# Optimization experiments

Measured on AMD Instinct MI355X. Metric: run time of the kernel, lower is better.

Reference implementation:

```python
import jax, jax.numpy as jnp
import numpy as np

TEMP = 1.0

def setup_inputs() -> dict:
    key = jax.random.key(0)
    k1, k2, k3 = jax.random.split(key, 3)
    B, C, H, W = 8, 256, 64, 64
    h = jax.random.normal(k1, (B, C, H, W), dtype=jnp.float32)
    xs = jax.random.normal(k2, (B, C, H, W), dtype=jnp.float32)
    ys = jax.random.normal(k3, (B, C, H, W), dtype=jnp.float32)
    return {"h": h, "xs": xs, "ys": ys}

def reference(h, xs, ys):
    B, C, H, W = h.shape
    Bs, Cs, Hs, Ws = xs.shape
    hf = h.reshape(B, C, H * W)            # [B, C, N]   N = H*W
    xf = xs.reshape(Bs, Cs, Hs * Ws)       # [B, C, M]   M = Hs*Ws
    yf = ys.reshape(ys.shape[0], ys.shape[1], -1)  # [B, C, M]
    # attention[b, n, m] = sum_c h[b,c,n] * xs[b,c,m]
    attn = jnp.einsum('bcn,bcm->bnm', hf, xf)
    attn = jax.nn.softmax(attn / TEMP, axis=2)  # softmax over support positions m
    # xxs[b, c, n] = sum_m ys[b,c,m] * attn[b,n,m]
    xxs = jnp.einsum('bcm,bnm->bcn', yf, attn)
    return xxs.reshape(B, C, H, W)
```

## Files before the change

### kernel.cpp

```cpp
#include <hip/hip_runtime.h>
#include <stdint.h>

#define B_ 8
#define C_ 256
#define N_ 4096
#define M_ 4096
#define NT 64
#define MT 64
#define PP 72
#define L2E 1.44269504f

typedef _Float16 f16x8 __attribute__((ext_vector_type(8)));
typedef _Float16 f16x4 __attribute__((ext_vector_type(4)));
typedef float f32x4 __attribute__((ext_vector_type(4)));

__device__ __forceinline__ void async16(const _Float16* g, _Float16* l) {
    __builtin_amdgcn_global_load_lds(
        (const __attribute__((address_space(1))) void*)g,
        (__attribute__((address_space(3))) void*)l, 16, 0, 0);
}

__global__ __launch_bounds__(256) void kPre(const float* __restrict__ xs,
                                            const float* __restrict__ ys,
                                            _Float16* __restrict__ kt,
                                            _Float16* __restrict__ vb) {
    int bx = blockIdx.x;
    int t = threadIdx.x;
    if (bx < 2048) {
        __shared__ float tile[64][65];
        int b = bx >> 8, rem = bx & 255;
        int c0 = (rem >> 6) * 64, m0 = (rem & 63) * 64;
        int cl = t >> 4, m4 = (t & 15) * 4;
#pragma unroll
        for (int i = 0; i < 4; i++) {
            int c = c0 + cl + i * 16;
            const float4 v = *(const float4*)(xs + ((size_t)(b * C_ + c) * M_) + m0 + m4);
            tile[m4 + 0][cl + i * 16] = v.x;
            tile[m4 + 1][cl + i * 16] = v.y;
            tile[m4 + 2][cl + i * 16] = v.z;
            tile[m4 + 3][cl + i * 16] = v.w;
        }
        __syncthreads();
        int ml = t >> 4, c4 = (t & 15) * 4;
#pragma unroll
        for (int i = 0; i < 4; i++) {
            int m = m0 + ml + i * 16;
            f16x4 o;
            o[0] = (_Float16)tile[ml + i * 16][c4 + 0];
            o[1] = (_Float16)tile[ml + i * 16][c4 + 1];
            o[2] = (_Float16)tile[ml + i * 16][c4 + 2];
            o[3] = (_Float16)tile[ml + i * 16][c4 + 3];
            *(f16x4*)(kt + ((size_t)(b * M_ + m) * C_) + c0 + c4) = o;
        }
    } else {
        size_t i = ((size_t)(bx - 2048) * 256 + t) * 4;
        float4 v = *(const float4*)(ys + i);
        f16x4 o;
        o[0] = (_Float16)v.x; o[1] = (_Float16)v.y;
        o[2] = (_Float16)v.z; o[3] = (_Float16)v.w;
        *(f16x4*)(vb + i) = o;
    }
}

__global__ __launch_bounds__(256, 2) void kAttn(const float* __restrict__ h,
                                                const _Float16* __restrict__ kt,
                                                const _Float16* __restrict__ vb,
                                                float* __restrict__ out) {
    __shared__ _Float16 sK[2][MT * 256];
    __shared__ _Float16 sP[NT * PP];
    __shared__ float sAlpha[NT];
    __shared__ float sL[NT];
    __shared__ int sFlag[2];

    const int t = threadIdx.x;
    const int w = t >> 6, lane = t & 63, quad = lane >> 4, l15 = lane & 15;
    const int b = blockIdx.x >> 6;
    const int n0 = (blockIdx.x & 63) * NT;
    const int nb = w * 16;
    const int cb = w * 64;

    const _Float16* srcKb = kt + (size_t)b * M_ * C_;
    const _Float16* srcVb = vb + (size_t)b * C_ * M_;

    if (t == 0) { sFlag[0] = 0; sFlag[1] = 0; }

    {
        int cl = t >> 4, n4 = (t & 15) * 4;
        for (int i = 0; i < 16; i++) {
            int c = i * 16 + cl;
            const float4 v = *(const float4*)(h + ((size_t)(b * C_ + c) * N_) + n0 + n4);
            float xv[4] = {v.x, v.y, v.z, v.w};
#pragma unroll
            for (int j = 0; j < 4; j++) {
                int row = n4 + j;
                sK[1][row * 256 + (((c >> 3) ^ (row & 31)) << 3) + (c & 7)] = (_Float16)xv[j];
            }
        }
#pragma unroll
        for (int j = 0; j < 8; j++) {
            int row = w * 16 + j * 2 + (lane >> 5);
            int logi = (lane & 31) ^ (row & 31);
            async16(srcKb + (size_t)row * C_ + logi * 8, &sK[0][(w * 16 + j * 2) * 256]);
        }
    }
    asm volatile("s_waitcnt lgkmcnt(0)" ::: "memory");
    __builtin_amdgcn_s_barrier();

    f16x8 qf[8];
    {
        int qrow = nb + l15;
#pragma unroll
        for (int ks = 0; ks < 8; ks++)
            qf[ks] = *(const f16x8*)(&sK[1][qrow * 256 + ((((ks << 2) + quad) ^ (qrow & 31)) << 3)]);
    }
    asm volatile("s_waitcnt lgkmcnt(0)" ::: "memory");

    f32x4 o[4][4];
#pragma unroll
    for (int i = 0; i < 4; i++)
#pragma unroll
        for (int j = 0; j < 4; j++)
            o[i][j] = (f32x4){0.f, 0.f, 0.f, 0.f};

    float mst = -3.0e38f, lp = 0.f;

    for (int it = 0; it < M_ / MT; it++) {
        const int cur = it & 1, nxt = cur ^ 1;
        const int m0i = it * MT;
        asm volatile("s_waitcnt vmcnt(0)" ::: "memory");
        __builtin_amdgcn_s_barrier();

        if (t == 0) sFlag[nxt] = 0;

        f16x8 vf[2][4];
#pragma unroll
        for (int ks = 0; ks < 2; ks++)
#pragma unroll
            for (int ct = 0; ct < 4; ct++) {
                int vrow = cb + ct * 16 + l15;
                vf[ks][ct] = *(const f16x8*)(srcVb + (size_t)vrow * M_ + m0i + ks * 32 + quad * 8);
            }
        __builtin_amdgcn_sched_barrier(0);

        if (it + 1 < M_ / MT) {
            const _Float16* srcK = srcKb + (size_t)(m0i + MT) * C_;
#pragma unroll
            for (int j = 0; j < 8; j++) {
                int row = w * 16 + j * 2 + (lane >> 5);
                int logi = (lane & 31) ^ (row & 31);
                async16(srcK + (size_t)row * C_ + logi * 8, &sK[nxt][(w * 16 + j * 2) * 256]);
            }
        }

        f32x4 s[4];
#pragma unroll
        for (int mt = 0; mt < 4; mt++) s[mt] = (f32x4){0.f, 0.f, 0.f, 0.f};
        __builtin_amdgcn_s_setprio(1);
#pragma unroll
        for (int ks = 0; ks < 8; ks++) {
#pragma unroll
            for (int mt = 0; mt < 4; mt++) {
                int krow = mt * 16 + l15;
                f16x8 bk = *(const f16x8*)(&sK[cur][krow * 256 + ((((ks << 2) + quad) ^ (krow & 31)) << 3)]);
                s[mt] = __builtin_amdgcn_mfma_f32_16x16x32_f16(bk, qf[ks], s[mt], 0, 0, 0);
            }
        }
        __builtin_amdgcn_s_setprio(0);

        float rowmax = fmaxf(fmaxf(fmaxf(s[0][0], s[0][1]), fmaxf(s[0][2], s[0][3])),
                             fmaxf(fmaxf(s[1][0], s[1][1]), fmaxf(s[1][2], s[1][3])));
        rowmax = fmaxf(rowmax, fmaxf(fmaxf(fmaxf(s[2][0], s[2][1]), fmaxf(s[2][2], s[2][3])),
                                     fmaxf(fmaxf(s[3][0], s[3][1]), fmaxf(s[3][2], s[3][3]))));
        rowmax = fmaxf(rowmax, __shfl_xor(rowmax, 16, 64));
        rowmax = fmaxf(rowmax, __shfl_xor(rowmax, 32, 64));
        float al = 1.0f;
        if (rowmax > mst) {
            al = exp2f((mst - rowmax) * L2E);
            mst = rowmax;
        }
        const float mb = mst * L2E;
        float psum = 0.f;
#pragma unroll
        for (int mt = 0; mt < 4; mt++)
#pragma unroll
            for (int r = 0; r < 4; r++) {
                float p = exp2f(s[mt][r] * L2E - mb);
                s[mt][r] = p;
                psum += p;
            }
        lp = lp * al + psum;
        if (quad == 0) {
            sAlpha[nb + l15] = al;
            if (al != 1.0f) atomicOr(&sFlag[cur], 1);
        }
#pragma unroll
        for (int mt = 0; mt < 4; mt++) {
            f16x4 pk;
            pk[0] = (_Float16)s[mt][0];
            pk[1] = (_Float16)s[mt][1];
            pk[2] = (_Float16)s[mt][2];
            pk[3] = (_Float16)s[mt][3];
            *(f16x4*)(&sP[(nb + l15) * PP + mt * 16 + quad * 4]) = pk;
        }

        asm volatile("s_waitcnt lgkmcnt(0)" ::: "memory");
        __builtin_amdgcn_s_barrier();

        if (sFlag[cur]) {
            float av[4];
#pragma unroll
            for (int nt = 0; nt < 4; nt++) av[nt] = sAlpha[nt * 16 + l15];
#pragma unroll
            for (int ct = 0; ct < 4; ct++)
#pragma unroll
                for (int nt = 0; nt < 4; nt++) {
                    o[ct][nt][0] *= av[nt];
                    o[ct][nt][1] *= av[nt];
                    o[ct][nt][2] *= av[nt];
                    o[ct][nt][3] *= av[nt];
                }
        }

        __builtin_amdgcn_s_setprio(1);
#pragma unroll
        for (int ks = 0; ks < 2; ks++) {
#pragma unroll
            for (int nt = 0; nt < 4; nt++) {
                f16x8 bp = *(const f16x8*)(sP + (nt * 16 + l15) * PP + ks * 32 + quad * 8);
#pragma unroll
                for (int ct = 0; ct < 4; ct++)
                    o[ct][nt] = __builtin_amdgcn_mfma_f32_16x16x32_f16(vf[ks][ct], bp, o[ct][nt], 0, 0, 0);
            }
        }
        __builtin_amdgcn_s_setprio(0);
    }

    lp += __shfl_xor(lp, 16, 64);
    lp += __shfl_xor(lp, 32, 64);
    if (quad == 0) sL[nb + l15] = lp;
    __syncthreads();
    float linv[4];
#pragma unroll
    for (int nt = 0; nt < 4; nt++) linv[nt] = 1.0f / sL[nt * 16 + l15];
#pragma unroll
    for (int ct = 0; ct < 4; ct++)
#pragma unroll
        for (int nt = 0; nt < 4; nt++)
#pragma unroll
            for (int r = 0; r < 4; r++) {
                int c = cb + ct * 16 + quad * 4 + r;
                out[((size_t)(b * C_ + c)) * N_ + n0 + nt * 16 + l15] = o[ct][nt][r] * linv[nt];
            }
}

extern "C" void kernel_launch(void* const* d_in, const int* in_sizes, int n_in,
                              void* d_out, int out_size, void* d_ws, size_t ws_size,
                              hipStream_t stream) {
    const float* h  = (const float*)d_in[0];
    const float* xs = (const float*)d_in[1];
    const float* ys = (const float*)d_in[2];
    float* out = (float*)d_out;

    _Float16* kt  = (_Float16*)d_ws;
    _Float16* vbb = kt + (size_t)B_ * M_ * C_;

    kPre<<<dim3(2048 + 8192), 256, 0, stream>>>(xs, ys, kt, vbb);
    kAttn<<<dim3(B_ * (N_ / NT)), 256, 0, stream>>>(h, kt, vbb, out);
}
```

Measured before the change: 361.2 us.

## Split attention into producer and consumer waves with one-step software pipeline

Doubles the block to 8 waves: four waves compute QK^T scores and online softmax for a 32-key tile while four other waves apply rescaling and the PV MFMA for the previous tile. Q is moved from registers to LDS, the key tile shrinks from 64 to 32, and the block-to-batch mapping is interleaved. The intent is to overlap softmax/score work with the PV accumulation and raise occupancy, at the cost of twice as many barriers per key and more LDS pressure.

Result: slower. 503.5 us (+39.4%).

```diff
diff --git a/kernel.cpp b/kernel.cpp
--- a/kernel.cpp
+++ b/kernel.cpp
@@ -6,8 +6,9 @@
 #define N_ 4096
 #define M_ 4096
 #define NT 64
-#define MT 64
-#define PP 72
+#define MT 32
+#define MITER (M_ / MT)
+#define PP 40
 #define L2E 1.44269504f
 
 typedef _Float16 f16x8 __attribute__((ext_vector_type(8)));
@@ -62,11 +63,12 @@
     }
 }
 
-__global__ __launch_bounds__(256, 2) void kAttn(const float* __restrict__ h,
+__global__ __launch_bounds__(512, 4) void kAttn(const float* __restrict__ h,
                                                 const _Float16* __restrict__ kt,
                                                 const _Float16* __restrict__ vb,
                                                 float* __restrict__ out) {
     __shared__ _Float16 sK[2][MT * 256];
+    __shared__ _Float16 sQ[NT * 256];
     __shared__ _Float16 sP[NT * PP];
     __shared__ float sAlpha[NT];
     __shared__ float sL[NT];
@@ -74,46 +76,39 @@
 
     const int t = threadIdx.x;
     const int w = t >> 6, lane = t & 63, quad = lane >> 4, l15 = lane & 15;
-    const int b = blockIdx.x >> 6;
-    const int n0 = (blockIdx.x & 63) * NT;
-    const int nb = w * 16;
-    const int cb = w * 64;
+    const int b = blockIdx.x & 7;
+    const int n0 = (blockIdx.x >> 3) * NT;
+    const bool prod = (w < 4);
+    const int pw = w & 3;
+    const int nb = pw * 16;
+    const int cb = pw * 64;
 
     const _Float16* srcKb = kt + (size_t)b * M_ * C_;
     const _Float16* srcVb = vb + (size_t)b * C_ * M_;
 
     if (t == 0) { sFlag[0] = 0; sFlag[1] = 0; }
 
+#pragma unroll
+    for (int j = 0; j < 2; j++) {
+        int row = w * 4 + j * 2 + (lane >> 5);
+        int logi = (lane & 31) ^ (row & 31);
+        async16(srcKb + (size_t)row * C_ + logi * 8, &sK[0][(w * 4 + j * 2) * 256]);
+    }
     {
-        int cl = t >> 4, n4 = (t & 15) * 4;
-        for (int i = 0; i < 16; i++) {
-            int c = i * 16 + cl;
+        int cl = t >> 4;
+        int n4 = (t & 15) * 4;
+#pragma unroll
+        for (int i = 0; i < 8; i++) {
+            int c = i * 32 + cl;
             const float4 v = *(const float4*)(h + ((size_t)(b * C_ + c) * N_) + n0 + n4);
             float xv[4] = {v.x, v.y, v.z, v.w};
 #pragma unroll
             for (int j = 0; j < 4; j++) {
                 int row = n4 + j;
-                sK[1][row * 256 + (((c >> 3) ^ (row & 31)) << 3) + (c & 7)] = (_Float16)xv[j];
-            }
-        }
-#pragma unroll
-        for (int j = 0; j < 8; j++) {
-            int row = w * 16 + j * 2 + (lane >> 5);
-            int logi = (lane & 31) ^ (row & 31);
-            async16(srcKb + (size_t)row * C_ + logi * 8, &sK[0][(w * 16 + j * 2) * 256]);
-        }
-    }
-    asm volatile("s_waitcnt lgkmcnt(0)" ::: "memory");
-    __builtin_amdgcn_s_barrier();
-
-    f16x8 qf[8];
-    {
-        int qrow = nb + l15;
-#pragma unroll
-        for (int ks = 0; ks < 8; ks++)
-            qf[ks] = *(const f16x8*)(&sK[1][qrow * 256 + ((((ks << 2) + quad) ^ (qrow & 31)) << 3)]);
-    }
-    asm volatile("s_waitcnt lgkmcnt(0)" ::: "memory");
+                sQ[row * 256 + (((c >> 3) ^ (row & 31)) << 3) + (c & 7)] = (_Float16)xv[j];
+            }
+        }
+    }
 
     f32x4 o[4][4];
 #pragma unroll
@@ -121,136 +116,143 @@
 #pragma unroll
         for (int j = 0; j < 4; j++)
             o[i][j] = (f32x4){0.f, 0.f, 0.f, 0.f};
-
+    f16x8 vf[4];
     float mst = -3.0e38f, lp = 0.f;
-
-    for (int it = 0; it < M_ / MT; it++) {
+    float al = 1.0f;
+    f32x4 s4[2];
+
+    for (int it = 0; it <= MITER; it++) {
         const int cur = it & 1, nxt = cur ^ 1;
-        const int m0i = it * MT;
-        asm volatile("s_waitcnt vmcnt(0)" ::: "memory");
+        asm volatile("s_waitcnt vmcnt(0) lgkmcnt(0)" ::: "memory");
         __builtin_amdgcn_s_barrier();
 
-        if (t == 0) sFlag[nxt] = 0;
-
-        f16x8 vf[2][4];
-#pragma unroll
-        for (int ks = 0; ks < 2; ks++)
-#pragma unroll
-            for (int ct = 0; ct < 4; ct++) {
-                int vrow = cb + ct * 16 + l15;
-                vf[ks][ct] = *(const f16x8*)(srcVb + (size_t)vrow * M_ + m0i + ks * 32 + quad * 8);
-            }
-        __builtin_amdgcn_sched_barrier(0);
-
-        if (it + 1 < M_ / MT) {
-            const _Float16* srcK = srcKb + (size_t)(m0i + MT) * C_;
-#pragma unroll
-            for (int j = 0; j < 8; j++) {
-                int row = w * 16 + j * 2 + (lane >> 5);
+        if (it < MITER - 1) {
+            const _Float16* srcK = srcKb + (size_t)(it + 1) * MT * C_;
+#pragma unroll
+            for (int j = 0; j < 2; j++) {
+                int row = w * 4 + j * 2 + (lane >> 5);
                 int logi = (lane & 31) ^ (row & 31);
-                async16(srcK + (size_t)row * C_ + logi * 8, &sK[nxt][(w * 16 + j * 2) * 256]);
-            }
-        }
-
-        f32x4 s[4];
-#pragma unroll
-        for (int mt = 0; mt < 4; mt++) s[mt] = (f32x4){0.f, 0.f, 0.f, 0.f};
-        __builtin_amdgcn_s_setprio(1);
-#pragma unroll
-        for (int ks = 0; ks < 8; ks++) {
-#pragma unroll
-            for (int mt = 0; mt < 4; mt++) {
-                int krow = mt * 16 + l15;
-                f16x8 bk = *(const f16x8*)(&sK[cur][krow * 256 + ((((ks << 2) + quad) ^ (krow & 31)) << 3)]);
-                s[mt] = __builtin_amdgcn_mfma_f32_16x16x32_f16(bk, qf[ks], s[mt], 0, 0, 0);
-            }
-        }
-        __builtin_amdgcn_s_setprio(0);
-
-        float rowmax = fmaxf(fmaxf(fmaxf(s[0][0], s[0][1]), fmaxf(s[0][2], s[0][3])),
-                             fmaxf(fmaxf(s[1][0], s[1][1]), fmaxf(s[1][2], s[1][3])));
-        rowmax = fmaxf(rowmax, fmaxf(fmaxf(fmaxf(s[2][0], s[2][1]), fmaxf(s[2][2], s[2][3])),
-                                     fmaxf(fmaxf(s[3][0], s[3][1]), fmaxf(s[3][2], s[3][3]))));
-        rowmax = fmaxf(rowmax, __shfl_xor(rowmax, 16, 64));
-        rowmax = fmaxf(rowmax, __shfl_xor(rowmax, 32, 64));
-        float al = 1.0f;
-        if (rowmax > mst) {
-            al = exp2f((mst - rowmax) * L2E);
-            mst = rowmax;
-        }
-        const float mb = mst * L2E;
-        float psum = 0.f;
-#pragma unroll
-        for (int mt = 0; mt < 4; mt++)
-#pragma unroll
-            for (int r = 0; r < 4; r++) {
-                float p = exp2f(s[mt][r] * L2E - mb);
-                s[mt][r] = p;
-                psum += p;
-            }
-        lp = lp * al + psum;
-        if (quad == 0) {
-            sAlpha[nb + l15] = al;
-            if (al != 1.0f) atomicOr(&sFlag[cur], 1);
-        }
-#pragma unroll
-        for (int mt = 0; mt < 4; mt++) {
-            f16x4 pk;
-            pk[0] = (_Float16)s[mt][0];
-            pk[1] = (_Float16)s[mt][1];
-            pk[2] = (_Float16)s[mt][2];
-            pk[3] = (_Float16)s[mt][3];
-            *(f16x4*)(&sP[(nb + l15) * PP + mt * 16 + quad * 4]) = pk;
+                async16(srcK + (size_t)row * C_ + logi * 8, &sK[nxt][(w * 4 + j * 2) * 256]);
+            }
+        }
+
+        if (prod) {
+            if (it < MITER) {
+                s4[0] = (f32x4){0.f, 0.f, 0.f, 0.f};
+                s4[1] = (f32x4){0.f, 0.f, 0.f, 0.f};
+                const int qrow = nb + l15;
+                __builtin_amdgcn_s_setprio(1);
+#pragma unroll
+                for (int ks = 0; ks < 8; ks++) {
+                    f16x8 qk = *(const f16x8*)(&sQ[qrow * 256 + ((((ks << 2) + quad) ^ (qrow & 31)) << 3)]);
+#pragma unroll
+                    for (int mt = 0; mt < 2; mt++) {
+                        int krow = mt * 16 + l15;
+                        f16x8 bk = *(const f16x8*)(&sK[cur][krow * 256 + ((((ks << 2) + quad) ^ (krow & 31)) << 3)]);
+                        s4[mt] = __builtin_amdgcn_mfma_f32_16x16x32_f16(bk, qk, s4[mt], 0, 0, 0);
+                    }
+                }
+                __builtin_amdgcn_s_setprio(0);
+
+                float rowmax = fmaxf(fmaxf(fmaxf(s4[0][0], s4[0][1]), fmaxf(s4[0][2], s4[0][3])),
+                                     fmaxf(fmaxf(s4[1][0], s4[1][1]), fmaxf(s4[1][2], s4[1][3])));
+                rowmax = fmaxf(rowmax, __shfl_xor(rowmax, 16, 64));
+                rowmax = fmaxf(rowmax, __shfl_xor(rowmax, 32, 64));
+                al = 1.0f;
+                if (rowmax > mst) {
+                    al = exp2f((mst - rowmax) * L2E);
+                    mst = rowmax;
+                }
+                const float mb = mst * L2E;
+                float psum = 0.f;
+#pragma unroll
+                for (int mt = 0; mt < 2; mt++)
+#pragma unroll
+                    for (int r = 0; r < 4; r++) {
+                        float p = exp2f(s4[mt][r] * L2E - mb);
+                        s4[mt][r] = p;
+                        psum += p;
+                    }
+                lp = lp * al + psum;
+            }
+        } else {
+            if (it > 0 && sFlag[nxt]) {
+                float av[4];
+#pragma unroll
+                for (int nt = 0; nt < 4; nt++) av[nt] = sAlpha[nt * 16 + l15];
+#pragma unroll
+                for (int ct = 0; ct < 4; ct++)
+#pragma unroll
+                    for (int nt = 0; nt < 4; nt++) {
+                        o[ct][nt][0] *= av[nt];
+                        o[ct][nt][1] *= av[nt];
+                        o[ct][nt][2] *= av[nt];
+                        o[ct][nt][3] *= av[nt];
+                    }
+            }
+            if (it > 0) {
+                __builtin_amdgcn_s_setprio(1);
+#pragma unroll
+                for (int nt = 0; nt < 4; nt++) {
+                    f16x8 bp = *(const f16x8*)(sP + (nt * 16 + l15) * PP + quad * 8);
+#pragma unroll
+                    for (int ct = 0; ct < 4; ct++)
+                        o[ct][nt] = __builtin_amdgcn_mfma_f32_16x16x32_f16(vf[ct], bp, o[ct][nt], 0, 0, 0);
+                }
+                __builtin_amdgcn_s_setprio(0);
+            }
+            if (it < MITER) {
+                int m0i = it * MT;
+#pragma unroll
+                for (int ct = 0; ct < 4; ct++) {
+                    int vrow = cb + ct * 16 + l15;
+                    vf[ct] = *(const f16x8*)(srcVb + (size_t)vrow * M_ + m0i + quad * 8);
+                }
+            }
         }
 
         asm volatile("s_waitcnt lgkmcnt(0)" ::: "memory");
         __builtin_amdgcn_s_barrier();
 
-        if (sFlag[cur]) {
-            float av[4];
-#pragma unroll
-            for (int nt = 0; nt < 4; nt++) av[nt] = sAlpha[nt * 16 + l15];
-#pragma unroll
-            for (int ct = 0; ct < 4; ct++)
-#pragma unroll
-                for (int nt = 0; nt < 4; nt++) {
-                    o[ct][nt][0] *= av[nt];
-                    o[ct][nt][1] *= av[nt];
-                    o[ct][nt][2] *= av[nt];
-                    o[ct][nt][3] *= av[nt];
-                }
-        }
-
-        __builtin_amdgcn_s_setprio(1);
-#pragma unroll
-        for (int ks = 0; ks < 2; ks++) {
-#pragma unroll
-            for (int nt = 0; nt < 4; nt++) {
-                f16x8 bp = *(const f16x8*)(sP + (nt * 16 + l15) * PP + ks * 32 + quad * 8);
-#pragma unroll
-                for (int ct = 0; ct < 4; ct++)
-                    o[ct][nt] = __builtin_amdgcn_mfma_f32_16x16x32_f16(vf[ks][ct], bp, o[ct][nt], 0, 0, 0);
-            }
-        }
-        __builtin_amdgcn_s_setprio(0);
-    }
-
-    lp += __shfl_xor(lp, 16, 64);
-    lp += __shfl_xor(lp, 32, 64);
-    if (quad == 0) sL[nb + l15] = lp;
+        if (prod && it < MITER) {
+            int prow = nb + l15;
+#pragma unroll
+            for (int mt = 0; mt < 2; mt++) {
+                f16x4 pk;
+                pk[0] = (_Float16)s4[mt][0];
+                pk[1] = (_Float16)s4[mt][1];
+                pk[2] = (_Float16)s4[mt][2];
+                pk[3] = (_Float16)s4[mt][3];
+                *(f16x4*)(&sP[prow * PP + mt * 16 + quad * 4]) = pk;
+            }
+            if (quad == 0) {
+                sAlpha[prow] = al;
+                if (al != 1.0f) atomicOr(&sFlag[cur], 1);
+            }
+            if (t == 0) sFlag[nxt] = 0;
+        }
+    }
+
+    if (prod) {
+        lp += __shfl_xor(lp, 16, 64);
+        lp += __shfl_xor(lp, 32, 64);
+        if (quad == 0) sL[nb + l15] = lp;
+    }
     __syncthreads();
-    float linv[4];
-#pragma unroll
-    for (int nt = 0; nt < 4; nt++) linv[nt] = 1.0f / sL[nt * 16 + l15];
-#pragma unroll
-    for (int ct = 0; ct < 4; ct++)
-#pragma unroll
-        for (int nt = 0; nt < 4; nt++)
-#pragma unroll
-            for (int r = 0; r < 4; r++) {
-                int c = cb + ct * 16 + quad * 4 + r;
-                out[((size_t)(b * C_ + c)) * N_ + n0 + nt * 16 + l15] = o[ct][nt][r] * linv[nt];
-            }
+    if (!prod) {
+        float linv[4];
+#pragma unroll
+        for (int nt = 0; nt < 4; nt++) linv[nt] = 1.0f / sL[nt * 16 + l15];
+#pragma unroll
+        for (int ct = 0; ct < 4; ct++)
+#pragma unroll
+            for (int nt = 0; nt < 4; nt++)
+#pragma unroll
+                for (int r = 0; r < 4; r++) {
+                    int c = cb + ct * 16 + quad * 4 + r;
+                    out[((size_t)(b * C_ + c)) * N_ + n0 + nt * 16 + l15] = o[ct][nt][r] * linv[nt];
+                }
+    }
 }
 
 extern "C" void kernel_launch(void* const* d_in, const int* in_sizes, int n_in,
@@ -265,5 +267,5 @@
     _Float16* vbb = kt + (size_t)B_ * M_ * C_;
 
     kPre<<<dim3(2048 + 8192), 256, 0, stream>>>(xs, ys, kt, vbb);
-    kAttn<<<dim3(B_ * (N_ / NT)), 256, 0, stream>>>(h, kt, vbb, out);
-}
+    kAttn<<<dim3(B_ * (N_ / NT)), 512, 0, stream>>>(h, kt, vbb, out);
+}
```
